# Performance work log

Hardware: AMD Instinct MI355X
Metric: run time of the kernel (lower is better)

Reference implementation:

```python
import jax, jax.numpy as jnp
import numpy as np
from jax import lax

BETA = 0.25            # commitment_beta (multiplies code_book_loss per source)
CODEBOOK_WEIGHT = 1.0  # multiplies commitment_loss per source
GN_GROUPS = 8
GN_EPS = 1e-5


def conv2d(x, w, b):
    # 3x3 same-padding conv, NCHW / OIHW
    y = lax.conv_general_dilated(x, w, (1, 1), [(1, 1), (1, 1)],
                                 dimension_numbers=('NCHW', 'OIHW', 'NCHW'))
    return y + b[None, :, None, None]


def group_norm(x, scale, bias):
    B, C, H, W = x.shape
    xg = x.reshape(B, GN_GROUPS, C // GN_GROUPS, H, W)
    mean = xg.mean(axis=(2, 3, 4), keepdims=True)
    var = xg.var(axis=(2, 3, 4), keepdims=True)
    xg = (xg - mean) * lax.rsqrt(var + GN_EPS)
    x = xg.reshape(B, C, H, W)
    return x * scale[None, :, None, None] + bias[None, :, None, None]


def setup_inputs() -> dict:
    key = jax.random.key(0)
    ks = jax.random.split(key, 4)
    x = jax.random.normal(ks[0], (8, 3, 64, 64), jnp.float32)
    conv_in_w = jax.random.normal(ks[1], (64, 3, 3, 3), jnp.float32) * 0.1
    conv_in_b = jnp.zeros((64,), jnp.float32)
    codebook = jax.random.normal(ks[2], (4096, 64), jnp.float32) * 0.5
    gn_scale = jnp.ones((64,), jnp.float32)
    gn_bias = jnp.zeros((64,), jnp.float32)
    dec_w = jax.random.normal(ks[3], (3, 64, 3, 3), jnp.float32) * 0.1
    dec_b = jnp.zeros((3,), jnp.float32)
    return {"x": x, "conv_in_w": conv_in_w, "conv_in_b": conv_in_b,
            "codebook": codebook, "gn_scale": gn_scale, "gn_bias": gn_bias,
            "dec_w": dec_w, "dec_b": dec_b}


def reference(x, conv_in_w, conv_in_b, codebook, gn_scale, gn_bias, dec_w, dec_b):
    # Encoder: channels=[64], mid_layers=[64] => just conv_in
    feat = conv2d(x, conv_in_w, conv_in_b)          # [B,64,H,W]
    B, C, H, W = feat.shape

    # quantize(): cdist -> argmin -> gather -> losses -> straight-through
    quant_in = feat.transpose(0, 2, 3, 1).reshape(B, H * W, C)  # [B,n,C]
    # squared euclidean distances (argmin identical to torch.cdist p=2 argmin)
    d = ((quant_in ** 2).sum(-1, keepdims=True)
         - 2.0 * jnp.einsum('bnc,kc->bnk', quant_in, codebook)
         + (codebook ** 2).sum(-1)[None, None, :])              # [B,n,K]
    min_idx = jnp.argmin(d, axis=-1)                            # [B,n]
    quant_out = codebook[min_idx.reshape(-1)]                   # [B*n,C]
    qi_flat = quant_in.reshape(-1, C)                            # [B*n,C]

    commitment_loss = CODEBOOK_WEIGHT * jnp.mean(
        (lax.stop_gradient(quant_out) - qi_flat) ** 2)
    code_book_loss = BETA * jnp.mean(
        (lax.stop_gradient(qi_flat) - quant_out) ** 2)

    st = qi_flat + lax.stop_gradient(quant_out - qi_flat)        # straight-through
    quant_nchw = st.reshape(B, H, W, C).transpose(0, 3, 1, 2)

    # Decoder: channels=[64] => norm_out + silu + decoder_out
    out = group_norm(quant_nchw, gn_scale, gn_bias)
    out = jax.nn.silu(out)
    reconstruction = conv2d(out, dec_w, dec_b)                   # [B,3,H,W]
    return reconstruction, quant_nchw, commitment_loss, code_book_loss
```

## Files before the change

### kernel.cpp

```cpp
#include <hip/hip_runtime.h>
#include <hip/hip_bf16.h>

typedef __attribute__((ext_vector_type(8))) short short8;
typedef __attribute__((ext_vector_type(4))) float f32x4;

#define KK 4096
#define NELEM 2097152
#define TAU 2.5e-4f

__device__ __forceinline__ unsigned short f2bf(float f) {
    unsigned u = __float_as_uint(f);
    u = (u + 0x7FFFu + ((u >> 16) & 1u)) >> 16;
    return (unsigned short)u;
}
__device__ __forceinline__ float bf2f(unsigned short h) {
    return __uint_as_float(((unsigned)h) << 16);
}

__global__ void k_prep(const float* __restrict__ cb, float* __restrict__ cn,
                       unsigned short* __restrict__ cbh, unsigned short* __restrict__ cbl,
                       int* __restrict__ wszero) {
    if (blockIdx.x == 0) {
        for (int i = threadIdx.x; i < 256; i += 256) wszero[i] = 0;
    }
    int t = blockIdx.x * 256 + threadIdx.x;
    int row = t >> 2, part = t & 3;
    const float4* p = (const float4*)(cb + (size_t)row * 64 + part * 16);
    float s = 0.f;
    short8 hv[2], lv[2];
#pragma unroll
    for (int i = 0; i < 4; i++) {
        float4 v = p[i];
        float arr[4] = {v.x, v.y, v.z, v.w};
#pragma unroll
        for (int j = 0; j < 4; j++) {
            float f = arr[j];
            s += f * f;
            int e = i * 4 + j;
            unsigned short h = f2bf(f);
            hv[e >> 3][e & 7] = (short)h;
            lv[e >> 3][e & 7] = (short)f2bf(f - bf2f(h));
        }
    }
    short8* oh = (short8*)(cbh + (size_t)row * 64 + part * 16);
    short8* ol = (short8*)(cbl + (size_t)row * 64 + part * 16);
    oh[0] = hv[0]; oh[1] = hv[1];
    ol[0] = lv[0]; ol[1] = lv[1];
    s += __shfl_xor(s, 1, 64);
    s += __shfl_xor(s, 2, 64);
    if (part == 0) cn[row] = s;
}

#define MFMA __builtin_amdgcn_mfma_f32_16x16x32_bf16

__global__ __launch_bounds__(256, 2) void k_argmin(
    const float* __restrict__ x, const float* __restrict__ ciw, const float* __restrict__ cib,
    const unsigned short* __restrict__ cbh, const unsigned short* __restrict__ cbl,
    const float* __restrict__ cn, const float* __restrict__ cb,
    float* __restrict__ quant, float* __restrict__ ssd,
    float* __restrict__ gsum, float* __restrict__ gsq) {

    __shared__ float    slab[3][3][66];
    __shared__ unsigned qtile[64][65];
    __shared__ float    qf32[64][65];
    __shared__ float    mb1[4][64];
    __shared__ float    mb2[4][64];
    __shared__ int      mi1[4][64];
    __shared__ int      fi[64];
    __shared__ float    gred[4][16];
    __shared__ int      nflag;
    __shared__ int      flagged[64];
    __shared__ float    rb[4];
    __shared__ int      ri[4];

    const int tid = threadIdx.x;
    const int L   = tid & 63;
    const int wv  = tid >> 6;
    const int grp = blockIdx.x;
    const int b   = grp >> 6, h = grp & 63;

    if (tid == 0) nflag = 0;
    for (int idx = tid; idx < 594; idx += 256) {
        int ci = idx / 198, rem = idx - ci * 198;
        int kh = rem / 66,  colp = rem - kh * 66;
        int hh = h + kh - 1, ww = colp - 1;
        float v = 0.f;
        if (hh >= 0 && hh < 64 && ww >= 0 && ww < 64)
            v = x[((b * 3 + ci) << 12) + (hh << 6) + ww];
        slab[ci][kh][colp] = v;
    }
    __syncthreads();

    {
        const int w_  = L;
        const int cgs = __builtin_amdgcn_readfirstlane(wv);
        float xv[27];
#pragma unroll
        for (int ci = 0; ci < 3; ci++)
#pragma unroll
            for (int kh = 0; kh < 3; kh++)
#pragma unroll
                for (int kw = 0; kw < 3; kw++)
                    xv[ci * 9 + kh * 3 + kw] = slab[ci][kh][w_ + kw];
#pragma unroll
        for (int j = 0; j < 16; j++) {
            int co = cgs * 16 + j;
            float acc = cib[co];
#pragma unroll
            for (int t2 = 0; t2 < 27; t2++)
                acc = fmaf(xv[t2], ciw[co * 27 + t2], acc);
            unsigned short hbits = f2bf(acc);
            unsigned short lbits = f2bf(acc - bf2f(hbits));
            qf32[w_][co]  = acc;
            qtile[w_][co] = (unsigned)hbits | ((unsigned)lbits << 16);
        }
    }
    __syncthreads();

    const int col = L & 15, g = L >> 4;
    short8 qh[4][2], ql[4][2];
#pragma unroll
    for (int mt = 0; mt < 4; mt++) {
        int qrow = mt * 16 + col;
#pragma unroll
        for (int kh = 0; kh < 2; kh++) {
            int d0 = (kh * 4 + g) * 8;
#pragma unroll
            for (int e = 0; e < 8; e++) {
                unsigned u = qtile[qrow][d0 + e];
                qh[mt][kh][e] = (short)(u & 0xFFFFu);
                ql[mt][kh][e] = (short)(u >> 16);
            }
        }
    }

    float vb1[4][4], vb2[4][4];
    int   vi1[4][4];
#pragma unroll
    for (int mt = 0; mt < 4; mt++)
#pragma unroll
        for (int e = 0; e < 4; e++) { vb1[mt][e] = 3.4e38f; vb2[mt][e] = 3.4e38f; vi1[mt][e] = 0; }

    const int cbase0 = wv << 10;
    const unsigned short* ph = cbh + (size_t)(cbase0 + col) * 64;
    const unsigned short* pl = cbl + (size_t)(cbase0 + col) * 64;
    const float* pcn = cn + cbase0 + col;

    short8 c0h0, c0h1, c0l0, c0l1, c1h0, c1h1, c1l0, c1l1;
    float  cn0, cn1;

    auto LD = [&](int gi, short8& h0, short8& h1, short8& l0, short8& l1, float& cnv) {
        const short8* p0 = (const short8*)(ph + ((size_t)gi << 10));
        const short8* p1 = (const short8*)(pl + ((size_t)gi << 10));
        h0 = p0[g]; h1 = p0[4 + g]; l0 = p1[g]; l1 = p1[4 + g];
        cnv = pcn[gi << 4];
    };
    auto PROC = [&](int gi, short8& h0, short8& h1, short8& l0, short8& l1, float cnv) {
        int kvb = cbase0 + gi * 16 + col;
#pragma unroll
        for (int mt = 0; mt < 4; mt++) {
            f32x4 acc = {0.f, 0.f, 0.f, 0.f};
            acc = MFMA(qh[mt][0], h0, acc, 0, 0, 0);
            acc = MFMA(qh[mt][1], h1, acc, 0, 0, 0);
            acc = MFMA(qh[mt][0], l0, acc, 0, 0, 0);
            acc = MFMA(qh[mt][1], l1, acc, 0, 0, 0);
            acc = MFMA(ql[mt][0], h0, acc, 0, 0, 0);
            acc = MFMA(ql[mt][1], h1, acc, 0, 0, 0);
#pragma unroll
            for (int e = 0; e < 4; e++) {
                float s = fmaf(acc[e], -2.f, cnv);
                vb2[mt][e] = __builtin_amdgcn_fmed3f(s, vb1[mt][e], vb2[mt][e]);
                bool take = s < vb1[mt][e];
                vi1[mt][e] = take ? kvb : vi1[mt][e];
                vb1[mt][e] = take ? s : vb1[mt][e];
            }
        }
    };

    LD(0, c0h0, c0h1, c0l0, c0l1, cn0);
#pragma unroll 1
    for (int gi = 0; gi < 64; gi += 2) {
        LD(gi + 1, c1h0, c1h1, c1l0, c1l1, cn1);
        PROC(gi, c0h0, c0h1, c0l0, c0l1, cn0);
        int gn = gi + 2 <= 63 ? gi + 2 : 63;
        LD(gn, c0h0, c0h1, c0l0, c0l1, cn0);
        PROC(gi + 1, c1h0, c1h1, c1l0, c1l1, cn1);
    }

#pragma unroll
    for (int mt = 0; mt < 4; mt++)
#pragma unroll
    for (int e = 0; e < 4; e++) {
        float b1 = vb1[mt][e], b2 = vb2[mt][e];
        int i1 = vi1[mt][e];
#pragma unroll
        for (int m = 1; m < 16; m <<= 1) {
            float ob1 = __shfl_xor(b1, m, 64);
            float ob2 = __shfl_xor(b2, m, 64);
            int   oi1 = __shfl_xor(i1, m, 64);
            float hi = fmaxf(b1, ob1);
            b2 = fminf(fminf(b2, ob2), hi);
            bool take = (ob1 < b1) || ((ob1 == b1) && (oi1 < i1));
            if (take) { b1 = ob1; i1 = oi1; }
        }
        if (col == 0) {
            int qloc = mt * 16 + g * 4 + e;
            mb1[wv][qloc] = b1; mb2[wv][qloc] = b2; mi1[wv][qloc] = i1;
        }
    }
    __syncthreads();

    if (tid < 64) {
        float b1 = mb1[0][tid], b2 = mb2[0][tid];
        int i1 = mi1[0][tid];
#pragma unroll
        for (int w2 = 1; w2 < 4; w2++) {
            float ob1 = mb1[w2][tid], ob2 = mb2[w2][tid];
            int   oi1 = mi1[w2][tid];
            float hi = fmaxf(b1, ob1);
            b2 = fminf(fminf(b2, ob2), hi);
            bool take = (ob1 < b1) || ((ob1 == b1) && (oi1 < i1));
            if (take) { b1 = ob1; i1 = oi1; }
        }
        fi[tid] = i1;
        if (b2 - b1 < TAU) {
            int p = atomicAdd(&nflag, 1);
            flagged[p] = tid;
        }
    }
    __syncthreads();

    int nf = nflag;
    for (int r = 0; r < nf; r++) {
        int qf = flagged[r];
        float best = 3.4e38f; int bi = 0;
        for (int kk = 0; kk < 16; kk++) {
            int k = kk * 256 + tid;
            const float4* cp = (const float4*)(cb + (size_t)k * 64);
            float d0 = 0.f, d1 = 0.f, d2 = 0.f, d3 = 0.f;
#pragma unroll
            for (int i = 0; i < 16; i += 4) {
                float4 c0 = cp[i], c1 = cp[i+1], c2 = cp[i+2], c3 = cp[i+3];
                d0 += qf32[qf][4*i+ 0]*c0.x + qf32[qf][4*i+ 1]*c0.y + qf32[qf][4*i+ 2]*c0.z + qf32[qf][4*i+ 3]*c0.w;
                d1 += qf32[qf][4*i+ 4]*c1.x + qf32[qf][4*i+ 5]*c1.y + qf32[qf][4*i+ 6]*c1.z + qf32[qf][4*i+ 7]*c1.w;
                d2 += qf32[qf][4*i+ 8]*c2.x + qf32[qf][4*i+ 9]*c2.y + qf32[qf][4*i+10]*c2.z + qf32[qf][4*i+11]*c2.w;
                d3 += qf32[qf][4*i+12]*c3.x + qf32[qf][4*i+13]*c3.y + qf32[qf][4*i+14]*c3.z + qf32[qf][4*i+15]*c3.w;
            }
            float s = cn[k] - 2.f * ((d0 + d1) + (d2 + d3));
            if (s < best) { best = s; bi = k; }
        }
#pragma unroll
        for (int off = 32; off; off >>= 1) {
            float ob = __shfl_down(best, off, 64);
            int   oi = __shfl_down(bi, off, 64);
            if (ob < best || (ob == best && oi < bi)) { best = ob; bi = oi; }
        }
        if (L == 0) { rb[wv] = best; ri[wv] = bi; }
        __syncthreads();
        if (tid == 0) {
            float bb = rb[0]; int ii = ri[0];
#pragma unroll
            for (int w2 = 1; w2 < 4; w2++)
                if (rb[w2] < bb || (rb[w2] == bb && ri[w2] < ii)) { bb = rb[w2]; ii = ri[w2]; }
            fi[qf] = ii;
        }
        __syncthreads();
    }

    {
        int qloc = tid >> 2, part = tid & 3;
        int idx = fi[qloc];
        int q = (grp << 6) + qloc;
        int hw = q & 4095;
        const float* crow = cb + (size_t)idx * 64 + part * 16;
        float* qout = quant + ((size_t)b << 18) + ((size_t)(part * 16) << 12) + hw;
        float ps = 0.f, sA = 0.f, sA2 = 0.f, sB = 0.f, sB2 = 0.f;
#pragma unroll
        for (int cc = 0; cc < 16; cc++) {
            float fv = qf32[qloc][part * 16 + cc];
            float cv = crow[cc];
            float d = cv - fv;
            ps += d * d;
            if (cc < 8) { sA += cv; sA2 += cv * cv; } else { sB += cv; sB2 += cv * cv; }
            qout[(size_t)cc << 12] = cv;
        }
#pragma unroll
        for (int off = 32; off; off >>= 1) ps += __shfl_down(ps, off, 64);
        if (L == 0) atomicAdd(ssd, ps);
#pragma unroll
        for (int m = 4; m <= 32; m <<= 1) {
            sA  += __shfl_xor(sA, m, 64);  sA2 += __shfl_xor(sA2, m, 64);
            sB  += __shfl_xor(sB, m, 64);  sB2 += __shfl_xor(sB2, m, 64);
        }
        if (L < 4) {
            gred[wv][L * 4 + 0] = sA;  gred[wv][L * 4 + 1] = sA2;
            gred[wv][L * 4 + 2] = sB;  gred[wv][L * 4 + 3] = sB2;
        }
    }
    __syncthreads();
    if (tid < 16) {
        float v = gred[0][tid] + gred[1][tid] + gred[2][tid] + gred[3][tid];
        int part = tid >> 2, stat = tid & 3;
        int g2 = b * 8 + part * 2 + (stat >> 1);
        atomicAdd((stat & 1) ? &gsq[g2] : &gsum[g2], v);
    }
}

__global__ __launch_bounds__(256, 2) void k_out(
    const float* __restrict__ quant,
    const float* __restrict__ gsum, const float* __restrict__ gsq,
    const float* __restrict__ scale, const float* __restrict__ bias,
    const float* __restrict__ dw, const float* __restrict__ db,
    const float* __restrict__ ssd, float* __restrict__ losses,
    float* __restrict__ out) {

    __shared__ float nls[64 * 3 * 66];
    __shared__ float sc_s[64], bi_s[64];

    const int tid = threadIdx.x;
    const int blk = blockIdx.x;
    const int b = blk >> 6, h = blk & 63;

    if (blk == 0 && tid == 0) {
        float mean = ssd[0] / 2097152.f;
        losses[0] = mean;
        losses[1] = 0.25f * mean;
    }

    if (tid < 64) {
        int grp = b * 8 + (tid >> 3);
        float m = gsum[grp] * (1.f / 32768.f);
        float var = gsq[grp] * (1.f / 32768.f) - m * m;
        float r = rsqrtf(var + 1e-5f);
        float sc = scale[tid] * r;
        sc_s[tid] = sc;
        bi_s[tid] = bias[tid] - m * sc;
    }
    for (int idx = tid; idx < 384; idx += 256) {
        int ci = idx / 6, r2 = idx % 6;
        int kh = r2 >> 1, side = r2 & 1;
        nls[ci * 198 + kh * 66 + (side ? 65 : 0)] = 0.f;
    }
    __syncthreads();

#pragma unroll
    for (int i = 0; i < 48; i++) {
        int idx = tid + i * 256;
        int w_ = idx & 63;
        int t2 = idx >> 6;
        int kh = t2 % 3, ci = t2 / 3;
        int hh = h + kh - 1;
        float v = 0.f;
        if (hh >= 0 && hh < 64) {
            float qv = quant[((size_t)(b * 64 + ci) << 12) + (hh << 6) + w_];
            float y = qv * sc_s[ci] + bi_s[ci];
            v = y / (1.f + expf(-y));
        }
        nls[ci * 198 + kh * 66 + w_ + 1] = v;
    }
    __syncthreads();

    const int co = tid >> 6;
    const int w_ = tid & 63;
    if (co < 3) {
        float acc = db[co];
#pragma unroll 4
        for (int ci = 0; ci < 64; ci++) {
            const float* wt = dw + (size_t)(co * 64 + ci) * 9;
#pragma unroll
            for (int kh = 0; kh < 3; kh++) {
                const float* base = nls + ci * 198 + kh * 66 + w_;
                acc = fmaf(base[0], wt[kh * 3 + 0], acc);
                acc = fmaf(base[1], wt[kh * 3 + 1], acc);
                acc = fmaf(base[2], wt[kh * 3 + 2], acc);
            }
        }
        out[((size_t)(b * 3 + co) << 12) + (h << 6) + w_] = acc;
    }
}

extern "C" void kernel_launch(void* const* d_in, const int* in_sizes, int n_in,
                              void* d_out, int out_size, void* d_ws, size_t ws_size,
                              hipStream_t stream) {
    const float* x   = (const float*)d_in[0];
    const float* ciw = (const float*)d_in[1];
    const float* cib = (const float*)d_in[2];
    const float* cb  = (const float*)d_in[3];
    const float* gsc = (const float*)d_in[4];
    const float* gbi = (const float*)d_in[5];
    const float* dw  = (const float*)d_in[6];
    const float* db  = (const float*)d_in[7];

    float* out = (float*)d_out;
    char* wsb  = (char*)d_ws;

    float*          ssd  = (float*)wsb;
    float*          gsum = (float*)(wsb + 64);
    float*          gsq  = (float*)(wsb + 320);
    float*          cn   = (float*)(wsb + 4096);
    unsigned short* cbh  = (unsigned short*)(wsb + 131072);
    unsigned short* cbl  = (unsigned short*)(wsb + 655360);

    float* recon  = out;
    float* quant  = out + 98304;
    float* losses = out + 98304 + NELEM;

    k_prep   <<<64,  256, 0, stream>>>(cb, cn, cbh, cbl, (int*)wsb);
    k_argmin <<<512, 256, 0, stream>>>(x, ciw, cib, cbh, cbl, cn, cb,
                                       quant, ssd, gsum, gsq);
    k_out    <<<512, 256, 0, stream>>>(quant, gsum, gsq, gsc, gbi, dw, db,
                                       ssd, losses, recon);
}
```

Measured before the change: 272.0 us.

## Split argmin blocks to half-rows of 32 queries, doubling grid size

Each argmin block now handles 32 query pixels (half an image row) instead of 64, and the grid is doubled to 1024 blocks. The conv, MFMA distance loop, reductions and the quant write and group-stat epilogue are re-indexed to match. The aim is more blocks to fill all compute units on the MI355X. The cost is that each block streams the full codebook for half as many queries, so total codebook reads double and MFMA reuse per load halves.

Measured after the change: 302.6 us. 1.11x slower.

```diff
diff --git a/kernel.cpp b/kernel.cpp
--- a/kernel.cpp
+++ b/kernel.cpp
@@ -61,23 +61,24 @@
     float* __restrict__ gsum, float* __restrict__ gsq) {
 
     __shared__ float    slab[3][3][66];
-    __shared__ unsigned qtile[64][65];
-    __shared__ float    qf32[64][65];
-    __shared__ float    mb1[4][64];
-    __shared__ float    mb2[4][64];
-    __shared__ int      mi1[4][64];
-    __shared__ int      fi[64];
+    __shared__ unsigned qtile[32][65];
+    __shared__ float    qf32[32][65];
+    __shared__ float    mb1[4][32];
+    __shared__ float    mb2[4][32];
+    __shared__ int      mi1[4][32];
+    __shared__ int      fi[32];
     __shared__ float    gred[4][16];
     __shared__ int      nflag;
-    __shared__ int      flagged[64];
+    __shared__ int      flagged[32];
     __shared__ float    rb[4];
     __shared__ int      ri[4];
 
-    const int tid = threadIdx.x;
-    const int L   = tid & 63;
-    const int wv  = tid >> 6;
-    const int grp = blockIdx.x;
-    const int b   = grp >> 6, h = grp & 63;
+    const int tid  = threadIdx.x;
+    const int L    = tid & 63;
+    const int wv   = tid >> 6;
+    const int blk  = blockIdx.x;
+    const int grp  = blk >> 1, half = blk & 1;
+    const int b    = grp >> 6, h = grp & 63;
 
     if (tid == 0) nflag = 0;
     for (int idx = tid; idx < 594; idx += 256) {
@@ -92,8 +93,9 @@
     __syncthreads();
 
     {
-        const int w_  = L;
-        const int cgs = __builtin_amdgcn_readfirstlane(wv);
+        const int w_  = tid & 31;
+        const int cg  = tid >> 5;
+        const int wgl = (half << 5) + w_;
         float xv[27];
 #pragma unroll
         for (int ci = 0; ci < 3; ci++)
@@ -101,10 +103,10 @@
             for (int kh = 0; kh < 3; kh++)
 #pragma unroll
                 for (int kw = 0; kw < 3; kw++)
-                    xv[ci * 9 + kh * 3 + kw] = slab[ci][kh][w_ + kw];
-#pragma unroll
-        for (int j = 0; j < 16; j++) {
-            int co = cgs * 16 + j;
+                    xv[ci * 9 + kh * 3 + kw] = slab[ci][kh][wgl + kw];
+#pragma unroll
+        for (int j = 0; j < 8; j++) {
+            int co = cg * 8 + j;
             float acc = cib[co];
 #pragma unroll
             for (int t2 = 0; t2 < 27; t2++)
@@ -118,9 +120,9 @@
     __syncthreads();
 
     const int col = L & 15, g = L >> 4;
-    short8 qh[4][2], ql[4][2];
-#pragma unroll
-    for (int mt = 0; mt < 4; mt++) {
+    short8 qh[2][2], ql[2][2];
+#pragma unroll
+    for (int mt = 0; mt < 2; mt++) {
         int qrow = mt * 16 + col;
 #pragma unroll
         for (int kh = 0; kh < 2; kh++) {
@@ -134,10 +136,10 @@
         }
     }
 
-    float vb1[4][4], vb2[4][4];
-    int   vi1[4][4];
-#pragma unroll
-    for (int mt = 0; mt < 4; mt++)
+    float vb1[2][4], vb2[2][4];
+    int   vi1[2][4];
+#pragma unroll
+    for (int mt = 0; mt < 2; mt++)
 #pragma unroll
         for (int e = 0; e < 4; e++) { vb1[mt][e] = 3.4e38f; vb2[mt][e] = 3.4e38f; vi1[mt][e] = 0; }
 
@@ -158,7 +160,7 @@
     auto PROC = [&](int gi, short8& h0, short8& h1, short8& l0, short8& l1, float cnv) {
         int kvb = cbase0 + gi * 16 + col;
 #pragma unroll
-        for (int mt = 0; mt < 4; mt++) {
+        for (int mt = 0; mt < 2; mt++) {
             f32x4 acc = {0.f, 0.f, 0.f, 0.f};
             acc = MFMA(qh[mt][0], h0, acc, 0, 0, 0);
             acc = MFMA(qh[mt][1], h1, acc, 0, 0, 0);
@@ -188,7 +190,7 @@
     }
 
 #pragma unroll
-    for (int mt = 0; mt < 4; mt++)
+    for (int mt = 0; mt < 2; mt++)
 #pragma unroll
     for (int e = 0; e < 4; e++) {
         float b1 = vb1[mt][e], b2 = vb2[mt][e];
@@ -210,7 +212,7 @@
     }
     __syncthreads();
 
-    if (tid < 64) {
+    if (tid < 32) {
         float b1 = mb1[0][tid], b2 = mb2[0][tid];
         int i1 = mi1[0][tid];
 #pragma unroll
@@ -268,41 +270,40 @@
     }
 
     {
-        int qloc = tid >> 2, part = tid & 3;
+        int qloc = tid >> 3, part = tid & 7;
         int idx = fi[qloc];
-        int q = (grp << 6) + qloc;
-        int hw = q & 4095;
-        const float* crow = cb + (size_t)idx * 64 + part * 16;
-        float* qout = quant + ((size_t)b << 18) + ((size_t)(part * 16) << 12) + hw;
-        float ps = 0.f, sA = 0.f, sA2 = 0.f, sB = 0.f, sB2 = 0.f;
-#pragma unroll
-        for (int cc = 0; cc < 16; cc++) {
-            float fv = qf32[qloc][part * 16 + cc];
+        int hw = (h << 6) + (half << 5) + qloc;
+        const float* crow = cb + (size_t)idx * 64 + part * 8;
+        float* qout = quant + ((size_t)b << 18) + ((size_t)(part * 8) << 12) + hw;
+        float ps = 0.f, sA = 0.f, sA2 = 0.f;
+#pragma unroll
+        for (int cc = 0; cc < 8; cc++) {
+            float fv = qf32[qloc][part * 8 + cc];
             float cv = crow[cc];
             float d = cv - fv;
             ps += d * d;
-            if (cc < 8) { sA += cv; sA2 += cv * cv; } else { sB += cv; sB2 += cv * cv; }
+            sA += cv; sA2 += cv * cv;
             qout[(size_t)cc << 12] = cv;
         }
 #pragma unroll
         for (int off = 32; off; off >>= 1) ps += __shfl_down(ps, off, 64);
         if (L == 0) atomicAdd(ssd, ps);
 #pragma unroll
-        for (int m = 4; m <= 32; m <<= 1) {
-            sA  += __shfl_xor(sA, m, 64);  sA2 += __shfl_xor(sA2, m, 64);
-            sB  += __shfl_xor(sB, m, 64);  sB2 += __shfl_xor(sB2, m, 64);
-        }
-        if (L < 4) {
-            gred[wv][L * 4 + 0] = sA;  gred[wv][L * 4 + 1] = sA2;
-            gred[wv][L * 4 + 2] = sB;  gred[wv][L * 4 + 3] = sB2;
+        for (int m = 8; m <= 32; m <<= 1) {
+            sA  += __shfl_xor(sA, m, 64);
+            sA2 += __shfl_xor(sA2, m, 64);
+        }
+        if (L < 8) {
+            gred[wv][L * 2 + 0] = sA;
+            gred[wv][L * 2 + 1] = sA2;
         }
     }
     __syncthreads();
     if (tid < 16) {
         float v = gred[0][tid] + gred[1][tid] + gred[2][tid] + gred[3][tid];
-        int part = tid >> 2, stat = tid & 3;
-        int g2 = b * 8 + part * 2 + (stat >> 1);
-        atomicAdd((stat & 1) ? &gsq[g2] : &gsum[g2], v);
+        int part = tid >> 1, stat = tid & 1;
+        int g2 = b * 8 + part;
+        atomicAdd(stat ? &gsq[g2] : &gsum[g2], v);
     }
 }
 
@@ -405,9 +406,9 @@
     float* quant  = out + 98304;
     float* losses = out + 98304 + NELEM;
 
-    k_prep   <<<64,  256, 0, stream>>>(cb, cn, cbh, cbl, (int*)wsb);
-    k_argmin <<<512, 256, 0, stream>>>(x, ciw, cib, cbh, cbl, cn, cb,
-                                       quant, ssd, gsum, gsq);
-    k_out    <<<512, 256, 0, stream>>>(quant, gsum, gsq, gsc, gbi, dw, db,
-                                       ssd, losses, recon);
-}
+    k_prep   <<<64,   256, 0, stream>>>(cb, cn, cbh, cbl, (int*)wsb);
+    k_argmin <<<1024, 256, 0, stream>>>(x, ciw, cib, cbh, cbl, cn, cb,
+                                        quant, ssd, gsum, gsq);
+    k_out    <<<512,  256, 0, stream>>>(quant, gsum, gsq, gsc, gbi, dw, db,
+                                        ssd, losses, recon);
+}
```
